# Optimization experiments

Hardware: AMD Instinct MI355X
Metric: run time of the kernel (lower is better)

The kernel has to match this reference:

```python
import jax, jax.numpy as jnp
import numpy as np

N = 100000      # nodes
E = 1600000     # directed edges (avg degree 16)
F_IN, H, C = 128, 64, 40
P_DROP = 0.4144


def gcn_conv(h, row, col, deg_inv_sqrt, W, b):
    # h: [N, d_in] -> [N, d_out]. Symmetric-normalized aggregation with self-loops
    # already folded into (row, col, deg_inv_sqrt).
    h = h @ W                                   # transform first (d_out small)
    norm = deg_inv_sqrt[row] * deg_inv_sqrt[col]  # [E+N]
    msg = h[row] * norm[:, None]                # gather + scale
    out = jax.ops.segment_sum(msg, col, num_segments=N)  # scatter-add
    return out + b


def setup_inputs() -> dict:
    key = jax.random.key(0)
    k1, k2, k3, k4 = jax.random.split(key, 4)
    x = jax.random.normal(k1, (N, F_IN), dtype=jnp.float32)
    edge_index = jax.random.randint(k2, (2, E), 0, N, dtype=jnp.int32)
    W1 = jax.random.normal(k3, (F_IN, H), dtype=jnp.float32) * (1.0 / np.sqrt(F_IN))
    b1 = jnp.zeros((H,), dtype=jnp.float32)
    W2 = jax.random.normal(k4, (H, C), dtype=jnp.float32) * (1.0 / np.sqrt(H))
    b2 = jnp.zeros((C,), dtype=jnp.float32)
    return {"x": x, "edge_index": edge_index, "W1": W1, "b1": b1, "W2": W2, "b2": b2}


def reference(x, edge_index, W1, b1, W2, b2):
    # add self-loops (GCNConv default)
    self_idx = jnp.arange(N, dtype=edge_index.dtype)
    row = jnp.concatenate([edge_index[0], self_idx])
    col = jnp.concatenate([edge_index[1], self_idx])
    deg = jax.ops.segment_sum(jnp.ones_like(col, dtype=x.dtype), col, num_segments=N)
    deg_inv_sqrt = jax.lax.rsqrt(jnp.maximum(deg, 1.0))  # deg >= 1 with self-loops

    h = gcn_conv(x, row, col, deg_inv_sqrt, W1, b1)
    h = jax.nn.relu(h)
    # dropout p=0.4144 with a fixed key (deterministic reference)
    keep = 1.0 - P_DROP
    mask = jax.random.bernoulli(jax.random.key(42), keep, h.shape)
    h = jnp.where(mask, h / keep, 0.0)
    h = gcn_conv(h, row, col, deg_inv_sqrt, W2, b2)
    return jax.nn.log_softmax(h, axis=1)
```

## Files before the change

kernel.cpp:

```cpp
#include <hip/hip_runtime.h>
#include <cstdint>
#include <cstddef>

#define NNODES 100000
#define NEDGES 1600000
#define FIN    128
#define HID    64
#define NCLS   40
#define BSH    9
#define BNODES (1 << BSH)
#define NBUCK  ((NNODES + BNODES - 1) >> BSH)
#define EPB    8192
#define NBINBLK ((NEDGES + EPB - 1) / EPB)
#define CSR_CAP 12288

typedef __attribute__((ext_vector_type(8))) short bf16x8;
typedef __attribute__((ext_vector_type(16))) float f32x16;

__device__ __forceinline__ uint32_t bf16rne(float f) {
  uint32_t u = __float_as_uint(f);
  return (u + 0x7fffu + ((u >> 16) & 1u)) >> 16;
}
__device__ __forceinline__ float bfu(ushort us) { return __uint_as_float(((uint32_t)us) << 16); }

__device__ __forceinline__ uint32_t rotl32(uint32_t x, uint32_t r) {
  return (x << r) | (x >> (32u - r));
}

__device__ __forceinline__ void threefry2x32(uint32_t k0, uint32_t k1,
                                             uint32_t c0, uint32_t c1,
                                             uint32_t& o0, uint32_t& o1) {
  const uint32_t ks2 = k0 ^ k1 ^ 0x1BD11BDAu;
  uint32_t x0 = c0 + k0;
  uint32_t x1 = c1 + k1;
#define TF_R(r) { x0 += x1; x1 = rotl32(x1, r); x1 ^= x0; }
  TF_R(13u) TF_R(15u) TF_R(26u) TF_R(6u)
  x0 += k1;  x1 += ks2 + 1u;
  TF_R(17u) TF_R(29u) TF_R(16u) TF_R(24u)
  x0 += ks2; x1 += k0 + 2u;
  TF_R(13u) TF_R(15u) TF_R(26u) TF_R(6u)
  x0 += k0;  x1 += k1 + 3u;
  TF_R(17u) TF_R(29u) TF_R(16u) TF_R(24u)
  x0 += k1;  x1 += ks2 + 4u;
  TF_R(13u) TF_R(15u) TF_R(26u) TF_R(6u)
  x0 += ks2; x1 += k0 + 5u;
#undef TF_R
  o0 = x0; o1 = x1;
}

__global__ __launch_bounds__(256) void k_initcur(int* __restrict__ gcur) {
  gcur[threadIdx.x] = threadIdx.x * CSR_CAP;
}

__global__ __launch_bounds__(256) void k_bin(const int* __restrict__ row,
                                             const int* __restrict__ col,
                                             int* __restrict__ gcur,
                                             uint32_t* __restrict__ pairs) {
  __shared__ int hcnt[256];
  __shared__ int sc[256];
  __shared__ int lofs[256];
  __shared__ int cur2[256];
  __shared__ int gofs[256];
  __shared__ uint32_t buf[EPB];
  __shared__ unsigned char bid[EPB];
  const int t = threadIdx.x;
  const int e0 = blockIdx.x * EPB;
  const int m = min(EPB, NEDGES - e0);
  hcnt[t] = 0;
  __syncthreads();
  for (int i = t; i < m; i += 256) {
    atomicAdd(&hcnt[col[e0 + i] >> BSH], 1);
  }
  __syncthreads();
  sc[t] = hcnt[t];
  __syncthreads();
  for (int d = 1; d < 256; d <<= 1) {
    int u = (t >= d) ? sc[t - d] : 0;
    __syncthreads();
    sc[t] += u;
    __syncthreads();
  }
  const int ex = sc[t] - hcnt[t];
  lofs[t] = ex;
  cur2[t] = ex;
  if (t < NBUCK) gofs[t] = atomicAdd(&gcur[t], hcnt[t]);
  __syncthreads();
  for (int i = t; i < m; i += 256) {
    const int c = col[e0 + i];
    const int r = row[e0 + i];
    const int b = c >> BSH;
    const int p = atomicAdd(&cur2[b], 1);
    buf[p] = ((uint32_t)r << BSH) | (uint32_t)(c & (BNODES - 1));
    bid[p] = (unsigned char)b;
  }
  __syncthreads();
  for (int i = t; i < m; i += 256) {
    const int b = bid[i];
    pairs[gofs[b] + (i - lofs[b])] = buf[i];
  }
}

__global__ __launch_bounds__(256) void k_bscan(const int* __restrict__ gcur,
                                               int* __restrict__ bbase) {
  __shared__ int sc[256];
  __shared__ int cval[256];
  const int t = threadIdx.x;
  const int c = gcur[t] - t * CSR_CAP;
  cval[t] = c;
  sc[t] = c;
  __syncthreads();
  for (int d = 1; d < 256; d <<= 1) {
    int u = (t >= d) ? sc[t - d] : 0;
    __syncthreads();
    sc[t] += u;
    __syncthreads();
  }
  bbase[t] = sc[t] - cval[t];
}

__global__ __launch_bounds__(256) void k_csr(const uint32_t* __restrict__ pairs,
                                             const int* __restrict__ gcur,
                                             const int* __restrict__ bbase,
                                             int* __restrict__ offs,
                                             float* __restrict__ dis,
                                             int* __restrict__ elist) {
  __shared__ int hist[BNODES];
  __shared__ int ncur[BNODES];
  __shared__ int wsum[4];
  __shared__ int ebuf[CSR_CAP];
  const int b = blockIdx.x, t = threadIdx.x;
  const int nf = b << BSH;
  const int slot0 = b * CSR_CAP;
  const int ne = gcur[b] - slot0;
  const int base = bbase[b];
  hist[2 * t] = 0;
  hist[2 * t + 1] = 0;
  __syncthreads();
  for (int i = t; i < ne; i += 256) {
    atomicAdd(&hist[pairs[slot0 + i] & (BNODES - 1)], 1);
  }
  __syncthreads();
  const int a = hist[2 * t], c = hist[2 * t + 1];
  const int s = a + c;
  const int lane = t & 63, wid = t >> 6;
  int scv = s;
#pragma unroll
  for (int off = 1; off < 64; off <<= 1) {
    int u = __shfl_up(scv, off, 64);
    if (lane >= off) scv += u;
  }
  if (lane == 63) wsum[wid] = scv;
  __syncthreads();
  int wadd = 0;
  for (int w = 0; w < wid; ++w) wadd += wsum[w];
  const int ex = scv - s + wadd;
  const int n0 = nf + 2 * t, n1 = nf + 2 * t + 1;
  if (n0 < NNODES) {
    offs[n0] = base + ex;
    dis[n0] = rsqrtf((float)(a + 1));
  }
  if (n1 < NNODES) {
    offs[n1] = base + ex + a;
    dis[n1] = rsqrtf((float)(c + 1));
  }
  if (b == NBUCK - 1 && t == 0) offs[NNODES] = base + ne;
  ncur[2 * t] = ex;
  ncur[2 * t + 1] = ex + a;
  __syncthreads();
  for (int i = t; i < ne; i += 256) {
    const uint32_t p = pairs[slot0 + i];
    const int n = (int)(p & (BNODES - 1));
    const int sl = atomicAdd(&ncur[n], 1);
    ebuf[sl] = (int)(p >> BSH);
  }
  __syncthreads();
  for (int i = t; i < ne; i += 256) elist[base + i] = ebuf[i];
}

__global__ __launch_bounds__(256) void k_mm1(const float* __restrict__ x,
                                             const float* __restrict__ W1,
                                             const float* __restrict__ dis,
                                             ushort* __restrict__ h1s) {
  __shared__ ushort wl[FIN * HID];
  const int t = threadIdx.x;
  for (int i = t; i < FIN * HID; i += 256) wl[i] = (ushort)bf16rne(W1[i]);
  __syncthreads();

  const int lane = t & 63;
  const int wglob = blockIdx.x * 4 + (t >> 6);
  const int r0 = wglob * 64;
  if (r0 >= NNODES) return;
  const int c0 = lane & 31;
  const int hi8 = (lane >> 5) * 8;

  bf16x8 wb0[8], wb1[8];
#pragma unroll
  for (int ks = 0; ks < 8; ++ks) {
#pragma unroll
    for (int i = 0; i < 8; ++i) {
      const int k = ks * 16 + hi8 + i;
      wb0[ks][i] = (short)wl[k * HID + c0];
      wb1[ks][i] = (short)wl[k * HID + 32 + c0];
    }
  }

  const int ra = min(r0 + c0, NNODES - 1);
  const int rb = min(r0 + 32 + c0, NNODES - 1);
  f32x16 acc00 = {0}, acc01 = {0}, acc10 = {0}, acc11 = {0};
#pragma unroll
  for (int ks = 0; ks < 8; ++ks) {
    const int k0 = ks * 16 + hi8;
    const float4 fa0 = *reinterpret_cast<const float4*>(x + (size_t)ra * FIN + k0);
    const float4 fa1 = *reinterpret_cast<const float4*>(x + (size_t)ra * FIN + k0 + 4);
    const float4 fb0 = *reinterpret_cast<const float4*>(x + (size_t)rb * FIN + k0);
    const float4 fb1 = *reinterpret_cast<const float4*>(x + (size_t)rb * FIN + k0 + 4);
    bf16x8 a0, a1;
    a0[0] = (short)bf16rne(fa0.x); a0[1] = (short)bf16rne(fa0.y);
    a0[2] = (short)bf16rne(fa0.z); a0[3] = (short)bf16rne(fa0.w);
    a0[4] = (short)bf16rne(fa1.x); a0[5] = (short)bf16rne(fa1.y);
    a0[6] = (short)bf16rne(fa1.z); a0[7] = (short)bf16rne(fa1.w);
    a1[0] = (short)bf16rne(fb0.x); a1[1] = (short)bf16rne(fb0.y);
    a1[2] = (short)bf16rne(fb0.z); a1[3] = (short)bf16rne(fb0.w);
    a1[4] = (short)bf16rne(fb1.x); a1[5] = (short)bf16rne(fb1.y);
    a1[6] = (short)bf16rne(fb1.z); a1[7] = (short)bf16rne(fb1.w);
    acc00 = __builtin_amdgcn_mfma_f32_32x32x16_bf16(a0, wb0[ks], acc00, 0, 0, 0);
    acc01 = __builtin_amdgcn_mfma_f32_32x32x16_bf16(a0, wb1[ks], acc01, 0, 0, 0);
    acc10 = __builtin_amdgcn_mfma_f32_32x32x16_bf16(a1, wb0[ks], acc10, 0, 0, 0);
    acc11 = __builtin_amdgcn_mfma_f32_32x32x16_bf16(a1, wb1[ks], acc11, 0, 0, 0);
  }

  const int rrb = 4 * (lane >> 5);
#pragma unroll
  for (int reg = 0; reg < 16; ++reg) {
    const int rr = (reg & 3) + 8 * (reg >> 2) + rrb;
    const int r_a = r0 + rr;
    const int r_b = r0 + 32 + rr;
    if (r_a < NNODES) {
      const float d = dis[r_a];
      h1s[(size_t)r_a * HID + c0]      = (ushort)bf16rne(acc00[reg] * d);
      h1s[(size_t)r_a * HID + 32 + c0] = (ushort)bf16rne(acc01[reg] * d);
    }
    if (r_b < NNODES) {
      const float d = dis[r_b];
      h1s[(size_t)r_b * HID + c0]      = (ushort)bf16rne(acc10[reg] * d);
      h1s[(size_t)r_b * HID + 32 + c0] = (ushort)bf16rne(acc11[reg] * d);
    }
  }
}

__global__ __launch_bounds__(256) void k_mm2(const ushort* __restrict__ h2,
                                             const float* __restrict__ W2,
                                             const float* __restrict__ dis,
                                             ushort* __restrict__ gs) {
  __shared__ ushort wl[HID * 64];
  const int t = threadIdx.x;
  for (int i = t; i < HID * 64; i += 256) {
    const int k = i >> 6, c = i & 63;
    wl[i] = (c < NCLS) ? (ushort)bf16rne(W2[k * NCLS + c]) : (ushort)0;
  }
  __syncthreads();

  const int lane = t & 63;
  const int wglob = blockIdx.x * 4 + (t >> 6);
  const int r0 = wglob * 64;
  if (r0 >= NNODES) return;
  const int c0 = lane & 31;
  const int hi8 = (lane >> 5) * 8;

  bf16x8 wb0[4], wb1[4];
#pragma unroll
  for (int ks = 0; ks < 4; ++ks) {
#pragma unroll
    for (int i = 0; i < 8; ++i) {
      const int k = ks * 16 + hi8 + i;
      wb0[ks][i] = (short)wl[k * 64 + c0];
      wb1[ks][i] = (short)wl[k * 64 + 32 + c0];
    }
  }

  const int ra = min(r0 + c0, NNODES - 1);
  const int rb = min(r0 + 32 + c0, NNODES - 1);
  f32x16 acc00 = {0}, acc01 = {0}, acc10 = {0}, acc11 = {0};
#pragma unroll
  for (int ks = 0; ks < 4; ++ks) {
    const int k0 = ks * 16 + hi8;
    const bf16x8 a0 = *reinterpret_cast<const bf16x8*>(h2 + (size_t)ra * HID + k0);
    const bf16x8 a1 = *reinterpret_cast<const bf16x8*>(h2 + (size_t)rb * HID + k0);
    acc00 = __builtin_amdgcn_mfma_f32_32x32x16_bf16(a0, wb0[ks], acc00, 0, 0, 0);
    acc01 = __builtin_amdgcn_mfma_f32_32x32x16_bf16(a0, wb1[ks], acc01, 0, 0, 0);
    acc10 = __builtin_amdgcn_mfma_f32_32x32x16_bf16(a1, wb0[ks], acc10, 0, 0, 0);
    acc11 = __builtin_amdgcn_mfma_f32_32x32x16_bf16(a1, wb1[ks], acc11, 0, 0, 0);
  }

  const int rrb = 4 * (lane >> 5);
  const bool c1ok = c0 < (NCLS - 32);
#pragma unroll
  for (int reg = 0; reg < 16; ++reg) {
    const int rr = (reg & 3) + 8 * (reg >> 2) + rrb;
    const int r_a = r0 + rr;
    const int r_b = r0 + 32 + rr;
    if (r_a < NNODES) {
      const float d = dis[r_a];
      gs[(size_t)r_a * NCLS + c0] = (ushort)bf16rne(acc00[reg] * d);
      if (c1ok) gs[(size_t)r_a * NCLS + 32 + c0] = (ushort)bf16rne(acc01[reg] * d);
    }
    if (r_b < NNODES) {
      const float d = dis[r_b];
      gs[(size_t)r_b * NCLS + c0] = (ushort)bf16rne(acc10[reg] * d);
      if (c1ok) gs[(size_t)r_b * NCLS + 32 + c0] = (ushort)bf16rne(acc11[reg] * d);
    }
  }
}

__global__ __launch_bounds__(256) void k_agg1(const ushort* __restrict__ h1s,
                                              const int* __restrict__ elist,
                                              const int* __restrict__ offs,
                                              const float* __restrict__ dis,
                                              const float* __restrict__ b1,
                                              ushort* __restrict__ h2) {
  const int gid = blockIdx.x * 256 + threadIdx.x;
  const int node = gid >> 6;
  const int lane = gid & 63;
  if (node >= NNODES) return;
  const int base = offs[node];
  const int n = offs[node + 1] - base;
  float acc0 = bfu(h1s[(size_t)node * HID + lane]);
  float acc1 = 0.f, acc2 = 0.f, acc3 = 0.f;
  for (int k0 = 0; k0 < n; k0 += 64) {
    const int rem = n - k0;
    const int m = rem < 64 ? rem : 64;
    int src = 0;
    if (lane < m) src = elist[base + k0 + lane];
    int j = 0;
    for (; j + 4 <= m; j += 4) {
      const int s0 = __shfl(src, j, 64);
      const int s1 = __shfl(src, j + 1, 64);
      const int s2 = __shfl(src, j + 2, 64);
      const int s3 = __shfl(src, j + 3, 64);
      const float a0 = bfu(h1s[(size_t)s0 * HID + lane]);
      const float a1 = bfu(h1s[(size_t)s1 * HID + lane]);
      const float a2 = bfu(h1s[(size_t)s2 * HID + lane]);
      const float a3 = bfu(h1s[(size_t)s3 * HID + lane]);
      acc0 += a0; acc1 += a1; acc2 += a2; acc3 += a3;
    }
    for (; j < m; ++j) {
      const int s0 = __shfl(src, j, 64);
      acc0 += bfu(h1s[(size_t)s0 * HID + lane]);
    }
  }
  const float acc = (acc0 + acc1) + (acc2 + acc3);
  float v = acc * dis[node] + b1[lane];
  v = fmaxf(v, 0.0f);
  const uint32_t idx = (uint32_t)node * HID + lane;
  uint32_t o0, o1;
  threefry2x32(0u, 42u, 0u, idx, o0, o1);
  const uint32_t bits = o0 ^ o1;
  const float u = __uint_as_float((bits >> 9) | 0x3f800000u) - 1.0f;
  const float keepf = (float)(1.0 - 0.4144);
  const float val = (u < keepf) ? v / keepf : 0.0f;
  h2[idx] = (ushort)bf16rne(val);
}

__global__ __launch_bounds__(256) void k_agg2(const ushort* __restrict__ gs,
                                              const int* __restrict__ elist,
                                              const int* __restrict__ offs,
                                              const float* __restrict__ dis,
                                              const float* __restrict__ b2,
                                              float* __restrict__ out) {
  const int gid = blockIdx.x * 256 + threadIdx.x;
  const int node = gid >> 6;
  const int lane = gid & 63;
  if (node >= NNODES) return;
  const int base = offs[node];
  const int n = offs[node + 1] - base;
  float acc0 = (lane < NCLS) ? bfu(gs[(size_t)node * NCLS + lane]) : 0.0f;
  float acc1 = 0.f, acc2 = 0.f, acc3 = 0.f;
  for (int k0 = 0; k0 < n; k0 += 64) {
    const int rem = n - k0;
    const int m = rem < 64 ? rem : 64;
    int src = 0;
    if (lane < m) src = elist[base + k0 + lane];
    int j = 0;
    for (; j + 4 <= m; j += 4) {
      const int s0 = __shfl(src, j, 64);
      const int s1 = __shfl(src, j + 1, 64);
      const int s2 = __shfl(src, j + 2, 64);
      const int s3 = __shfl(src, j + 3, 64);
      const float a0 = bfu(gs[(size_t)s0 * NCLS + lane]);
      const float a1 = bfu(gs[(size_t)s1 * NCLS + lane]);
      const float a2 = bfu(gs[(size_t)s2 * NCLS + lane]);
      const float a3 = bfu(gs[(size_t)s3 * NCLS + lane]);
      if (lane < NCLS) { acc0 += a0; acc1 += a1; acc2 += a2; acc3 += a3; }
    }
    for (; j < m; ++j) {
      const int s0 = __shfl(src, j, 64);
      if (lane < NCLS) acc0 += bfu(gs[(size_t)s0 * NCLS + lane]);
    }
  }
  const float acc = (acc0 + acc1) + (acc2 + acc3);
  float v = (lane < NCLS) ? (acc * dis[node] + b2[lane]) : -INFINITY;
  float mx = v;
#pragma unroll
  for (int off = 32; off > 0; off >>= 1) mx = fmaxf(mx, __shfl_xor(mx, off, 64));
  float e = (lane < NCLS) ? expf(v - mx) : 0.0f;
  float s = e;
#pragma unroll
  for (int off = 32; off > 0; off >>= 1) s += __shfl_xor(s, off, 64);
  const float ls = logf(s);
  if (lane < NCLS) out[(size_t)node * NCLS + lane] = v - mx - ls;
}

extern "C" void kernel_launch(void* const* d_in, const int* in_sizes, int n_in,
                              void* d_out, int out_size, void* d_ws, size_t ws_size,
                              hipStream_t stream) {
  const float* x  = (const float*)d_in[0];
  const int*   ei = (const int*)d_in[1];
  const float* W1 = (const float*)d_in[2];
  const float* b1 = (const float*)d_in[3];
  const float* W2 = (const float*)d_in[4];
  const float* b2 = (const float*)d_in[5];
  float* out = (float*)d_out;

  const int* row = ei;
  const int* col = ei + NEDGES;

  float* ws  = (float*)d_ws;
  float* dis = ws;
  ushort* h1s = (ushort*)(ws + 100352);
  ushort* h2  = h1s + (size_t)NNODES * HID;
  int* offs  = (int*)(h2 + (size_t)NNODES * HID);
  int* gcur  = offs + NNODES + 64;
  int* bbase = gcur + 256;
  int* elist = bbase + 256;
  uint32_t* pairs = (uint32_t*)h1s;
  ushort* gs = h1s;

  const dim3 B(256);
  const int GNW = (NNODES * 64 + 255) / 256;
  const int GMM = (NNODES + 255) / 256;

  k_initcur<<<dim3(1), B, 0, stream>>>(gcur);
  k_bin  <<<dim3(NBINBLK), B, 0, stream>>>(row, col, gcur, pairs);
  k_bscan<<<dim3(1), B, 0, stream>>>(gcur, bbase);
  k_csr  <<<dim3(NBUCK), B, 0, stream>>>(pairs, gcur, bbase, offs, dis, elist);

  k_mm1 <<<dim3(GMM), B, 0, stream>>>(x, W1, dis, h1s);
  k_agg1<<<dim3(GNW), B, 0, stream>>>(h1s, elist, offs, dis, b1, h2);

  k_mm2 <<<dim3(GMM), B, 0, stream>>>(h2, W2, dis, gs);
  k_agg2<<<dim3(GNW), B, 0, stream>>>(gs, elist, offs, dis, b2, out);
}
```

Baseline: 205.2 us.

## Split feature tables into 16-wide column chunks and aggregate chunk by chunk

```diff
diff --git a/kernel.cpp b/kernel.cpp
--- a/kernel.cpp
+++ b/kernel.cpp
@@ -180,7 +180,7 @@
 __global__ __launch_bounds__(256) void k_mm1(const float* __restrict__ x,
                                              const float* __restrict__ W1,
                                              const float* __restrict__ dis,
-                                             ushort* __restrict__ h1s) {
+                                             ushort* __restrict__ h1c) {
   __shared__ ushort wl[FIN * HID];
   const int t = threadIdx.x;
   for (int i = t; i < FIN * HID; i += 256) wl[i] = (ushort)bf16rne(W1[i]);
@@ -230,6 +230,7 @@
   }
 
   const int rrb = 4 * (lane >> 5);
+  const int chA = c0 >> 4, flA = c0 & 15;
 #pragma unroll
   for (int reg = 0; reg < 16; ++reg) {
     const int rr = (reg & 3) + 8 * (reg >> 2) + rrb;
@@ -237,21 +238,21 @@
     const int r_b = r0 + 32 + rr;
     if (r_a < NNODES) {
       const float d = dis[r_a];
-      h1s[(size_t)r_a * HID + c0]      = (ushort)bf16rne(acc00[reg] * d);
-      h1s[(size_t)r_a * HID + 32 + c0] = (ushort)bf16rne(acc01[reg] * d);
+      h1c[((size_t)chA * NNODES + r_a) * 16 + flA]       = (ushort)bf16rne(acc00[reg] * d);
+      h1c[((size_t)(2 + chA) * NNODES + r_a) * 16 + flA] = (ushort)bf16rne(acc01[reg] * d);
     }
     if (r_b < NNODES) {
       const float d = dis[r_b];
-      h1s[(size_t)r_b * HID + c0]      = (ushort)bf16rne(acc10[reg] * d);
-      h1s[(size_t)r_b * HID + 32 + c0] = (ushort)bf16rne(acc11[reg] * d);
-    }
-  }
-}
-
-__global__ __launch_bounds__(256) void k_mm2(const ushort* __restrict__ h2,
+      h1c[((size_t)chA * NNODES + r_b) * 16 + flA]       = (ushort)bf16rne(acc10[reg] * d);
+      h1c[((size_t)(2 + chA) * NNODES + r_b) * 16 + flA] = (ushort)bf16rne(acc11[reg] * d);
+    }
+  }
+}
+
+__global__ __launch_bounds__(256) void k_mm2(const ushort* __restrict__ h2c,
                                              const float* __restrict__ W2,
                                              const float* __restrict__ dis,
-                                             ushort* __restrict__ gs) {
+                                             ushort* __restrict__ gs_c) {
   __shared__ ushort wl[HID * 64];
   const int t = threadIdx.x;
   for (int i = t; i < HID * 64; i += 256) {
@@ -283,9 +284,8 @@
   f32x16 acc00 = {0}, acc01 = {0}, acc10 = {0}, acc11 = {0};
 #pragma unroll
   for (int ks = 0; ks < 4; ++ks) {
-    const int k0 = ks * 16 + hi8;
-    const bf16x8 a0 = *reinterpret_cast<const bf16x8*>(h2 + (size_t)ra * HID + k0);
-    const bf16x8 a1 = *reinterpret_cast<const bf16x8*>(h2 + (size_t)rb * HID + k0);
+    const bf16x8 a0 = *reinterpret_cast<const bf16x8*>(h2c + ((size_t)ks * NNODES + ra) * 16 + hi8);
+    const bf16x8 a1 = *reinterpret_cast<const bf16x8*>(h2c + ((size_t)ks * NNODES + rb) * 16 + hi8);
     acc00 = __builtin_amdgcn_mfma_f32_32x32x16_bf16(a0, wb0[ks], acc00, 0, 0, 0);
     acc01 = __builtin_amdgcn_mfma_f32_32x32x16_bf16(a0, wb1[ks], acc01, 0, 0, 0);
     acc10 = __builtin_amdgcn_mfma_f32_32x32x16_bf16(a1, wb0[ks], acc10, 0, 0, 0);
@@ -293,7 +293,7 @@
   }
 
   const int rrb = 4 * (lane >> 5);
-  const bool c1ok = c0 < (NCLS - 32);
+  const int chA = c0 >> 4, flA = c0 & 15;
 #pragma unroll
   for (int reg = 0; reg < 16; ++reg) {
     const int rr = (reg & 3) + 8 * (reg >> 2) + rrb;
@@ -301,104 +301,122 @@
     const int r_b = r0 + 32 + rr;
     if (r_a < NNODES) {
       const float d = dis[r_a];
-      gs[(size_t)r_a * NCLS + c0] = (ushort)bf16rne(acc00[reg] * d);
-      if (c1ok) gs[(size_t)r_a * NCLS + 32 + c0] = (ushort)bf16rne(acc01[reg] * d);
+      gs_c[((size_t)chA * NNODES + r_a) * 16 + flA] = (ushort)bf16rne(acc00[reg] * d);
+      if (c0 < 8)       gs_c[((size_t)2 * NNODES + r_a) * 16 + c0] = (ushort)bf16rne(acc01[reg] * d);
+      else if (c0 < 16) gs_c[((size_t)2 * NNODES + r_a) * 16 + c0] = 0;
     }
     if (r_b < NNODES) {
       const float d = dis[r_b];
-      gs[(size_t)r_b * NCLS + c0] = (ushort)bf16rne(acc10[reg] * d);
-      if (c1ok) gs[(size_t)r_b * NCLS + 32 + c0] = (ushort)bf16rne(acc11[reg] * d);
-    }
-  }
-}
-
-__global__ __launch_bounds__(256) void k_agg1(const ushort* __restrict__ h1s,
-                                              const int* __restrict__ elist,
-                                              const int* __restrict__ offs,
-                                              const float* __restrict__ dis,
-                                              const float* __restrict__ b1,
-                                              ushort* __restrict__ h2) {
+      gs_c[((size_t)chA * NNODES + r_b) * 16 + flA] = (ushort)bf16rne(acc10[reg] * d);
+      if (c0 < 8)       gs_c[((size_t)2 * NNODES + r_b) * 16 + c0] = (ushort)bf16rne(acc11[reg] * d);
+      else if (c0 < 16) gs_c[((size_t)2 * NNODES + r_b) * 16 + c0] = 0;
+    }
+  }
+}
+
+__global__ __launch_bounds__(256) void k_agg1c(const ushort* __restrict__ h1c,
+                                               const int* __restrict__ elist,
+                                               const int* __restrict__ offs,
+                                               const float* __restrict__ dis,
+                                               const float* __restrict__ b1,
+                                               ushort* __restrict__ h2c,
+                                               int p) {
   const int gid = blockIdx.x * 256 + threadIdx.x;
   const int node = gid >> 6;
   const int lane = gid & 63;
   if (node >= NNODES) return;
+  const int q = lane >> 4, fl = lane & 15;
+  const ushort* tab = h1c + (size_t)p * NNODES * 16;
   const int base = offs[node];
   const int n = offs[node + 1] - base;
-  float acc0 = bfu(h1s[(size_t)node * HID + lane]);
+  float acc0 = (q == 0) ? bfu(tab[(size_t)node * 16 + fl]) : 0.f;
   float acc1 = 0.f, acc2 = 0.f, acc3 = 0.f;
   for (int k0 = 0; k0 < n; k0 += 64) {
-    const int rem = n - k0;
-    const int m = rem < 64 ? rem : 64;
-    int src = 0;
-    if (lane < m) src = elist[base + k0 + lane];
-    int j = 0;
-    for (; j + 4 <= m; j += 4) {
-      const int s0 = __shfl(src, j, 64);
-      const int s1 = __shfl(src, j + 1, 64);
-      const int s2 = __shfl(src, j + 2, 64);
-      const int s3 = __shfl(src, j + 3, 64);
-      const float a0 = bfu(h1s[(size_t)s0 * HID + lane]);
-      const float a1 = bfu(h1s[(size_t)s1 * HID + lane]);
-      const float a2 = bfu(h1s[(size_t)s2 * HID + lane]);
-      const float a3 = bfu(h1s[(size_t)s3 * HID + lane]);
-      acc0 += a0; acc1 += a1; acc2 += a2; acc3 += a3;
-    }
-    for (; j < m; ++j) {
-      const int s0 = __shfl(src, j, 64);
-      acc0 += bfu(h1s[(size_t)s0 * HID + lane]);
-    }
-  }
-  const float acc = (acc0 + acc1) + (acc2 + acc3);
-  float v = acc * dis[node] + b1[lane];
-  v = fmaxf(v, 0.0f);
-  const uint32_t idx = (uint32_t)node * HID + lane;
-  uint32_t o0, o1;
-  threefry2x32(0u, 42u, 0u, idx, o0, o1);
-  const uint32_t bits = o0 ^ o1;
-  const float u = __uint_as_float((bits >> 9) | 0x3f800000u) - 1.0f;
-  const float keepf = (float)(1.0 - 0.4144);
-  const float val = (u < keepf) ? v / keepf : 0.0f;
-  h2[idx] = (ushort)bf16rne(val);
-}
-
-__global__ __launch_bounds__(256) void k_agg2(const ushort* __restrict__ gs,
-                                              const int* __restrict__ elist,
-                                              const int* __restrict__ offs,
-                                              const float* __restrict__ dis,
-                                              const float* __restrict__ b2,
-                                              float* __restrict__ out) {
+    const int mm = min(64, n - k0);
+    int srcl = 0;
+    if (lane < mm) srcl = __builtin_nontemporal_load(elist + base + k0 + lane);
+    for (int j = 0; j < mm; j += 16) {
+      const int e0 = j + q, e1 = j + 4 + q, e2 = j + 8 + q, e3 = j + 12 + q;
+      const int s0 = __shfl(srcl, e0, 64);
+      const int s1 = __shfl(srcl, e1, 64);
+      const int s2 = __shfl(srcl, e2, 64);
+      const int s3 = __shfl(srcl, e3, 64);
+      if (e0 < mm) acc0 += bfu(tab[(size_t)s0 * 16 + fl]);
+      if (e1 < mm) acc1 += bfu(tab[(size_t)s1 * 16 + fl]);
+      if (e2 < mm) acc2 += bfu(tab[(size_t)s2 * 16 + fl]);
+      if (e3 < mm) acc3 += bfu(tab[(size_t)s3 * 16 + fl]);
+    }
+  }
+  float a = (acc0 + acc1) + (acc2 + acc3);
+  a += __shfl_xor(a, 16, 64);
+  a += __shfl_xor(a, 32, 64);
+  if (lane < 16) {
+    const int f = (p << 4) + fl;
+    float v = a * dis[node] + b1[f];
+    v = fmaxf(v, 0.0f);
+    const uint32_t idx = (uint32_t)node * HID + f;
+    uint32_t o0, o1;
+    threefry2x32(0u, 42u, 0u, idx, o0, o1);
+    const uint32_t bits = o0 ^ o1;
+    const float u = __uint_as_float((bits >> 9) | 0x3f800000u) - 1.0f;
+    const float keepf = (float)(1.0 - 0.4144);
+    const float val = (u < keepf) ? v / keepf : 0.0f;
+    h2c[((size_t)p * NNODES + node) * 16 + fl] = (ushort)bf16rne(val);
+  }
+}
+
+__global__ __launch_bounds__(256) void k_agg2c(const ushort* __restrict__ gs_c,
+                                               const int* __restrict__ elist,
+                                               const int* __restrict__ offs,
+                                               const float* __restrict__ dis,
+                                               const float* __restrict__ b2,
+                                               float* __restrict__ logits,
+                                               int p) {
   const int gid = blockIdx.x * 256 + threadIdx.x;
   const int node = gid >> 6;
   const int lane = gid & 63;
   if (node >= NNODES) return;
+  const int q = lane >> 4, fl = lane & 15;
+  const ushort* tab = gs_c + (size_t)p * NNODES * 16;
   const int base = offs[node];
   const int n = offs[node + 1] - base;
-  float acc0 = (lane < NCLS) ? bfu(gs[(size_t)node * NCLS + lane]) : 0.0f;
+  float acc0 = (q == 0) ? bfu(tab[(size_t)node * 16 + fl]) : 0.f;
   float acc1 = 0.f, acc2 = 0.f, acc3 = 0.f;
   for (int k0 = 0; k0 < n; k0 += 64) {
-    const int rem = n - k0;
-    const int m = rem < 64 ? rem : 64;
-    int src = 0;
-    if (lane < m) src = elist[base + k0 + lane];
-    int j = 0;
-    for (; j + 4 <= m; j += 4) {
-      const int s0 = __shfl(src, j, 64);
-      const int s1 = __shfl(src, j + 1, 64);
-      const int s2 = __shfl(src, j + 2, 64);
-      const int s3 = __shfl(src, j + 3, 64);
-      const float a0 = bfu(gs[(size_t)s0 * NCLS + lane]);
-      const float a1 = bfu(gs[(size_t)s1 * NCLS + lane]);
-      const float a2 = bfu(gs[(size_t)s2 * NCLS + lane]);
-      const float a3 = bfu(gs[(size_t)s3 * NCLS + lane]);
-      if (lane < NCLS) { acc0 += a0; acc1 += a1; acc2 += a2; acc3 += a3; }
-    }
-    for (; j < m; ++j) {
-      const int s0 = __shfl(src, j, 64);
-      if (lane < NCLS) acc0 += bfu(gs[(size_t)s0 * NCLS + lane]);
-    }
-  }
-  const float acc = (acc0 + acc1) + (acc2 + acc3);
-  float v = (lane < NCLS) ? (acc * dis[node] + b2[lane]) : -INFINITY;
+    const int mm = min(64, n - k0);
+    int srcl = 0;
+    if (lane < mm) srcl = __builtin_nontemporal_load(elist + base + k0 + lane);
+    for (int j = 0; j < mm; j += 16) {
+      const int e0 = j + q, e1 = j + 4 + q, e2 = j + 8 + q, e3 = j + 12 + q;
+      const int s0 = __shfl(srcl, e0, 64);
+      const int s1 = __shfl(srcl, e1, 64);
+      const int s2 = __shfl(srcl, e2, 64);
+      const int s3 = __shfl(srcl, e3, 64);
+      if (e0 < mm) acc0 += bfu(tab[(size_t)s0 * 16 + fl]);
+      if (e1 < mm) acc1 += bfu(tab[(size_t)s1 * 16 + fl]);
+      if (e2 < mm) acc2 += bfu(tab[(size_t)s2 * 16 + fl]);
+      if (e3 < mm) acc3 += bfu(tab[(size_t)s3 * 16 + fl]);
+    }
+  }
+  float a = (acc0 + acc1) + (acc2 + acc3);
+  a += __shfl_xor(a, 16, 64);
+  a += __shfl_xor(a, 32, 64);
+  if (lane < 16) {
+    const int f = (p << 4) + fl;
+    if (f < NCLS) logits[((size_t)p * NNODES + node) * 16 + fl] = a * dis[node] + b2[f];
+  }
+}
+
+__global__ __launch_bounds__(256) void k_lsm(const float* __restrict__ logits,
+                                             float* __restrict__ out) {
+  const int gid = blockIdx.x * 256 + threadIdx.x;
+  const int node = gid >> 6;
+  const int lane = gid & 63;
+  if (node >= NNODES) return;
+  float v = -INFINITY;
+  if (lane < NCLS) {
+    v = logits[((size_t)(lane >> 4) * NNODES + node) * 16 + (lane & 15)];
+  }
   float mx = v;
 #pragma unroll
   for (int off = 32; off > 0; off >>= 1) mx = fmaxf(mx, __shfl_xor(mx, off, 64));
@@ -426,14 +444,15 @@
 
   float* ws  = (float*)d_ws;
   float* dis = ws;
-  ushort* h1s = (ushort*)(ws + 100352);
-  ushort* h2  = h1s + (size_t)NNODES * HID;
-  int* offs  = (int*)(h2 + (size_t)NNODES * HID);
+  ushort* h1c = (ushort*)(ws + 100352);
+  ushort* h2c = h1c + (size_t)4 * NNODES * 16;
+  float* logits = (float*)(h2c + (size_t)4 * NNODES * 16);
+  int* offs  = (int*)(logits + (size_t)3 * NNODES * 16);
   int* gcur  = offs + NNODES + 64;
   int* bbase = gcur + 256;
   int* elist = bbase + 256;
-  uint32_t* pairs = (uint32_t*)h1s;
-  ushort* gs = h1s;
+  uint32_t* pairs = (uint32_t*)h2c;
+  ushort* gs_c = h1c;
 
   const dim3 B(256);
   const int GNW = (NNODES * 64 + 255) / 256;
@@ -444,9 +463,12 @@
   k_bscan<<<dim3(1), B, 0, stream>>>(gcur, bbase);
   k_csr  <<<dim3(NBUCK), B, 0, stream>>>(pairs, gcur, bbase, offs, dis, elist);
 
-  k_mm1 <<<dim3(GMM), B, 0, stream>>>(x, W1, dis, h1s);
-  k_agg1<<<dim3(GNW), B, 0, stream>>>(h1s, elist, offs, dis, b1, h2);
-
-  k_mm2 <<<dim3(GMM), B, 0, stream>>>(h2, W2, dis, gs);
-  k_agg2<<<dim3(GNW), B, 0, stream>>>(gs, elist, offs, dis, b2, out);
-}
+  k_mm1<<<dim3(GMM), B, 0, stream>>>(x, W1, dis, h1c);
+  for (int p = 0; p < 4; ++p)
+    k_agg1c<<<dim3(GNW), B, 0, stream>>>(h1c, elist, offs, dis, b1, h2c, p);
+
+  k_mm2<<<dim3(GMM), B, 0, stream>>>(h2c, W2, dis, gs_c);
+  for (int p = 0; p < 3; ++p)
+    k_agg2c<<<dim3(GNW), B, 0, stream>>>(gs_c, elist, offs, dis, b2, logits, p);
+  k_lsm<<<dim3(GNW), B, 0, stream>>>(logits, out);
+}
```

New measurement: 420.2 us. 2.05x slower.

## Vectorize aggregation gathers: eight edges per wave with 16-byte row loads

Applied to the files above, without the earlier changes.

```diff
diff --git a/kernel.cpp b/kernel.cpp
--- a/kernel.cpp
+++ b/kernel.cpp
@@ -21,7 +21,8 @@
   uint32_t u = __float_as_uint(f);
   return (u + 0x7fffu + ((u >> 16) & 1u)) >> 16;
 }
-__device__ __forceinline__ float bfu(ushort us) { return __uint_as_float(((uint32_t)us) << 16); }
+__device__ __forceinline__ float bflo(uint32_t u) { return __uint_as_float(u << 16); }
+__device__ __forceinline__ float bfhi(uint32_t u) { return __uint_as_float(u & 0xffff0000u); }
 
 __device__ __forceinline__ uint32_t rotl32(uint32_t x, uint32_t r) {
   return (x << r) | (x >> (32u - r));
@@ -293,7 +294,6 @@
   }
 
   const int rrb = 4 * (lane >> 5);
-  const bool c1ok = c0 < (NCLS - 32);
 #pragma unroll
   for (int reg = 0; reg < 16; ++reg) {
     const int rr = (reg & 3) + 8 * (reg >> 2) + rrb;
@@ -301,67 +301,75 @@
     const int r_b = r0 + 32 + rr;
     if (r_a < NNODES) {
       const float d = dis[r_a];
-      gs[(size_t)r_a * NCLS + c0] = (ushort)bf16rne(acc00[reg] * d);
-      if (c1ok) gs[(size_t)r_a * NCLS + 32 + c0] = (ushort)bf16rne(acc01[reg] * d);
+      gs[(size_t)r_a * 64 + c0]      = (ushort)bf16rne(acc00[reg] * d);
+      gs[(size_t)r_a * 64 + 32 + c0] = (ushort)bf16rne(acc01[reg] * d);
     }
     if (r_b < NNODES) {
       const float d = dis[r_b];
-      gs[(size_t)r_b * NCLS + c0] = (ushort)bf16rne(acc10[reg] * d);
-      if (c1ok) gs[(size_t)r_b * NCLS + 32 + c0] = (ushort)bf16rne(acc11[reg] * d);
-    }
-  }
-}
-
-__global__ __launch_bounds__(256) void k_agg1(const ushort* __restrict__ h1s,
+      gs[(size_t)r_b * 64 + c0]      = (ushort)bf16rne(acc10[reg] * d);
+      gs[(size_t)r_b * 64 + 32 + c0] = (ushort)bf16rne(acc11[reg] * d);
+    }
+  }
+}
+
+__global__ __launch_bounds__(256) void k_agg1(const uint32_t* __restrict__ h1u,
                                               const int* __restrict__ elist,
                                               const int* __restrict__ offs,
                                               const float* __restrict__ dis,
                                               const float* __restrict__ b1,
-                                              ushort* __restrict__ h2) {
+                                              ushort* __restrict__ h2s) {
   const int gid = blockIdx.x * 256 + threadIdx.x;
   const int node = gid >> 6;
   const int lane = gid & 63;
-  if (node >= NNODES) return;
+  const int q = lane >> 3, fl = lane & 7;
   const int base = offs[node];
   const int n = offs[node + 1] - base;
-  float acc0 = bfu(h1s[(size_t)node * HID + lane]);
-  float acc1 = 0.f, acc2 = 0.f, acc3 = 0.f;
+  float a0 = 0.f, a1 = 0.f, a2 = 0.f, a3 = 0.f, a4 = 0.f, a5 = 0.f, a6 = 0.f, a7 = 0.f;
+  if (q == 0) {
+    const uint4 u = *reinterpret_cast<const uint4*>(h1u + (size_t)node * 32 + fl * 4);
+    a0 = bflo(u.x); a1 = bfhi(u.x); a2 = bflo(u.y); a3 = bfhi(u.y);
+    a4 = bflo(u.z); a5 = bfhi(u.z); a6 = bflo(u.w); a7 = bfhi(u.w);
+  }
   for (int k0 = 0; k0 < n; k0 += 64) {
-    const int rem = n - k0;
-    const int m = rem < 64 ? rem : 64;
-    int src = 0;
-    if (lane < m) src = elist[base + k0 + lane];
-    int j = 0;
-    for (; j + 4 <= m; j += 4) {
-      const int s0 = __shfl(src, j, 64);
-      const int s1 = __shfl(src, j + 1, 64);
-      const int s2 = __shfl(src, j + 2, 64);
-      const int s3 = __shfl(src, j + 3, 64);
-      const float a0 = bfu(h1s[(size_t)s0 * HID + lane]);
-      const float a1 = bfu(h1s[(size_t)s1 * HID + lane]);
-      const float a2 = bfu(h1s[(size_t)s2 * HID + lane]);
-      const float a3 = bfu(h1s[(size_t)s3 * HID + lane]);
-      acc0 += a0; acc1 += a1; acc2 += a2; acc3 += a3;
-    }
-    for (; j < m; ++j) {
-      const int s0 = __shfl(src, j, 64);
-      acc0 += bfu(h1s[(size_t)s0 * HID + lane]);
-    }
-  }
-  const float acc = (acc0 + acc1) + (acc2 + acc3);
-  float v = acc * dis[node] + b1[lane];
-  v = fmaxf(v, 0.0f);
-  const uint32_t idx = (uint32_t)node * HID + lane;
+    const int m = min(64, n - k0);
+    int srcl = 0;
+    if (lane < m) srcl = elist[base + k0 + lane];
+    for (int j = 0; j < m; j += 8) {
+      const int e = j + q;
+      const int s = __shfl(srcl, e, 64);
+      if (e < m) {
+        const uint4 u = *reinterpret_cast<const uint4*>(h1u + (size_t)s * 32 + fl * 4);
+        a0 += bflo(u.x); a1 += bfhi(u.x); a2 += bflo(u.y); a3 += bfhi(u.y);
+        a4 += bflo(u.z); a5 += bfhi(u.z); a6 += bflo(u.w); a7 += bfhi(u.w);
+      }
+    }
+  }
+#pragma unroll
+  for (int off = 8; off < 64; off <<= 1) {
+    a0 += __shfl_xor(a0, off, 64); a1 += __shfl_xor(a1, off, 64);
+    a2 += __shfl_xor(a2, off, 64); a3 += __shfl_xor(a3, off, 64);
+    a4 += __shfl_xor(a4, off, 64); a5 += __shfl_xor(a5, off, 64);
+    a6 += __shfl_xor(a6, off, 64); a7 += __shfl_xor(a7, off, 64);
+  }
+  const int sl = lane >> 3;
+  const float v0 = __shfl(a0, sl, 64), v1 = __shfl(a1, sl, 64);
+  const float v2 = __shfl(a2, sl, 64), v3 = __shfl(a3, sl, 64);
+  const float v4 = __shfl(a4, sl, 64), v5 = __shfl(a5, sl, 64);
+  const float v6 = __shfl(a6, sl, 64), v7 = __shfl(a7, sl, 64);
+  const int ss = lane & 7;
+  float val = (ss == 0) ? v0 : (ss == 1) ? v1 : (ss == 2) ? v2 : (ss == 3) ? v3
+            : (ss == 4) ? v4 : (ss == 5) ? v5 : (ss == 6) ? v6 : v7;
+  float v = fmaxf(val * dis[node] + b1[lane], 0.0f);
   uint32_t o0, o1;
-  threefry2x32(0u, 42u, 0u, idx, o0, o1);
+  threefry2x32(0u, 42u, 0u, (uint32_t)node * HID + lane, o0, o1);
   const uint32_t bits = o0 ^ o1;
   const float u = __uint_as_float((bits >> 9) | 0x3f800000u) - 1.0f;
   const float keepf = (float)(1.0 - 0.4144);
-  const float val = (u < keepf) ? v / keepf : 0.0f;
-  h2[idx] = (ushort)bf16rne(val);
-}
-
-__global__ __launch_bounds__(256) void k_agg2(const ushort* __restrict__ gs,
+  const float r = (u < keepf) ? v / keepf : 0.0f;
+  h2s[(size_t)node * HID + lane] = (ushort)bf16rne(r);
+}
+
+__global__ __launch_bounds__(256) void k_agg2(const uint32_t* __restrict__ gsu,
                                               const int* __restrict__ elist,
                                               const int* __restrict__ offs,
                                               const float* __restrict__ dis,
@@ -370,44 +378,55 @@
   const int gid = blockIdx.x * 256 + threadIdx.x;
   const int node = gid >> 6;
   const int lane = gid & 63;
-  if (node >= NNODES) return;
+  const int q = lane >> 3, fl = lane & 7;
   const int base = offs[node];
   const int n = offs[node + 1] - base;
-  float acc0 = (lane < NCLS) ? bfu(gs[(size_t)node * NCLS + lane]) : 0.0f;
-  float acc1 = 0.f, acc2 = 0.f, acc3 = 0.f;
+  float a0 = 0.f, a1 = 0.f, a2 = 0.f, a3 = 0.f, a4 = 0.f, a5 = 0.f, a6 = 0.f, a7 = 0.f;
+  if (q == 0) {
+    const uint4 u = *reinterpret_cast<const uint4*>(gsu + (size_t)node * 32 + fl * 4);
+    a0 = bflo(u.x); a1 = bfhi(u.x); a2 = bflo(u.y); a3 = bfhi(u.y);
+    a4 = bflo(u.z); a5 = bfhi(u.z); a6 = bflo(u.w); a7 = bfhi(u.w);
+  }
   for (int k0 = 0; k0 < n; k0 += 64) {
-    const int rem = n - k0;
-    const int m = rem < 64 ? rem : 64;
-    int src = 0;
-    if (lane < m) src = elist[base + k0 + lane];
-    int j = 0;
-    for (; j + 4 <= m; j += 4) {
-      const int s0 = __shfl(src, j, 64);
-      const int s1 = __shfl(src, j + 1, 64);
-      const int s2 = __shfl(src, j + 2, 64);
-      const int s3 = __shfl(src, j + 3, 64);
-      const float a0 = bfu(gs[(size_t)s0 * NCLS + lane]);
-      const float a1 = bfu(gs[(size_t)s1 * NCLS + lane]);
-      const float a2 = bfu(gs[(size_t)s2 * NCLS + lane]);
-      const float a3 = bfu(gs[(size_t)s3 * NCLS + lane]);
-      if (lane < NCLS) { acc0 += a0; acc1 += a1; acc2 += a2; acc3 += a3; }
-    }
-    for (; j < m; ++j) {
-      const int s0 = __shfl(src, j, 64);
-      if (lane < NCLS) acc0 += bfu(gs[(size_t)s0 * NCLS + lane]);
-    }
-  }
-  const float acc = (acc0 + acc1) + (acc2 + acc3);
-  float v = (lane < NCLS) ? (acc * dis[node] + b2[lane]) : -INFINITY;
-  float mx = v;
+    const int m = min(64, n - k0);
+    int srcl = 0;
+    if (lane < m) srcl = elist[base + k0 + lane];
+    for (int j = 0; j < m; j += 8) {
+      const int e = j + q;
+      const int s = __shfl(srcl, e, 64);
+      if (e < m) {
+        const uint4 u = *reinterpret_cast<const uint4*>(gsu + (size_t)s * 32 + fl * 4);
+        a0 += bflo(u.x); a1 += bfhi(u.x); a2 += bflo(u.y); a3 += bfhi(u.y);
+        a4 += bflo(u.z); a5 += bfhi(u.z); a6 += bflo(u.w); a7 += bfhi(u.w);
+      }
+    }
+  }
+#pragma unroll
+  for (int off = 8; off < 64; off <<= 1) {
+    a0 += __shfl_xor(a0, off, 64); a1 += __shfl_xor(a1, off, 64);
+    a2 += __shfl_xor(a2, off, 64); a3 += __shfl_xor(a3, off, 64);
+    a4 += __shfl_xor(a4, off, 64); a5 += __shfl_xor(a5, off, 64);
+    a6 += __shfl_xor(a6, off, 64); a7 += __shfl_xor(a7, off, 64);
+  }
+  const int sl = lane >> 3;
+  const float v0 = __shfl(a0, sl, 64), v1 = __shfl(a1, sl, 64);
+  const float v2 = __shfl(a2, sl, 64), v3 = __shfl(a3, sl, 64);
+  const float v4 = __shfl(a4, sl, 64), v5 = __shfl(a5, sl, 64);
+  const float v6 = __shfl(a6, sl, 64), v7 = __shfl(a7, sl, 64);
+  const int ss = lane & 7;
+  float val = (ss == 0) ? v0 : (ss == 1) ? v1 : (ss == 2) ? v2 : (ss == 3) ? v3
+            : (ss == 4) ? v4 : (ss == 5) ? v5 : (ss == 6) ? v6 : v7;
+  const bool act = lane < NCLS;
+  const float l = act ? (val * dis[node] + b2[lane]) : -INFINITY;
+  float mx = l;
 #pragma unroll
   for (int off = 32; off > 0; off >>= 1) mx = fmaxf(mx, __shfl_xor(mx, off, 64));
-  float e = (lane < NCLS) ? expf(v - mx) : 0.0f;
+  float e = act ? expf(l - mx) : 0.0f;
   float s = e;
 #pragma unroll
   for (int off = 32; off > 0; off >>= 1) s += __shfl_xor(s, off, 64);
   const float ls = logf(s);
-  if (lane < NCLS) out[(size_t)node * NCLS + lane] = v - mx - ls;
+  if (act) out[(size_t)node * NCLS + lane] = l - mx - ls;
 }
 
 extern "C" void kernel_launch(void* const* d_in, const int* in_sizes, int n_in,
@@ -436,7 +455,7 @@
   ushort* gs = h1s;
 
   const dim3 B(256);
-  const int GNW = (NNODES * 64 + 255) / 256;
+  const int GNW = (NNODES * 64) / 256;
   const int GMM = (NNODES + 255) / 256;
 
   k_initcur<<<dim3(1), B, 0, stream>>>(gcur);
@@ -445,8 +464,8 @@
   k_csr  <<<dim3(NBUCK), B, 0, stream>>>(pairs, gcur, bbase, offs, dis, elist);
 
   k_mm1 <<<dim3(GMM), B, 0, stream>>>(x, W1, dis, h1s);
-  k_agg1<<<dim3(GNW), B, 0, stream>>>(h1s, elist, offs, dis, b1, h2);
+  k_agg1<<<dim3(GNW), B, 0, stream>>>((const uint32_t*)h1s, elist, offs, dis, b1, h2);
 
   k_mm2 <<<dim3(GMM), B, 0, stream>>>(h2, W2, dis, gs);
-  k_agg2<<<dim3(GNW), B, 0, stream>>>(gs, elist, offs, dis, b2, out);
-}
+  k_agg2<<<dim3(GNW), B, 0, stream>>>((const uint32_t*)gs, elist, offs, dis, b2, out);
+}
```

New measurement: 197.6 us (median of 2 runs). 1.04x faster.
